# Performance work log

Measured on AMD Instinct MI355X. Metric: run time of the kernel, lower is better.

Reference implementation:

```python
import jax, jax.numpy as jnp
import numpy as np

N_RAYS = 65536
N_COARSE = 64
N_FINE = 128


def setup_inputs() -> dict:
    key = jax.random.key(0)
    k0, k1, k2 = jax.random.split(key, 3)
    origins = jax.random.normal(k0, (N_RAYS, 3), dtype=jnp.float32)
    directions = jax.random.normal(k1, (N_RAYS, 3), dtype=jnp.float32)
    near = jnp.full((N_RAYS,), 2.0, dtype=jnp.float32)
    far = jnp.full((N_RAYS,), 6.0, dtype=jnp.float32)
    # coarse-pass weights used for inverse-CDF (PDF) fine sampling
    weights = jax.random.uniform(k2, (N_RAYS, N_COARSE), dtype=jnp.float32)
    return {"origins": origins, "directions": directions, "near": near,
            "far": far, "weights": weights}


def sample_pdf(bins, weights, n_samples):
    """Inverse-CDF sampling. bins: [N, B], weights: [N, B-1] -> [N, n_samples]."""
    w = weights + 1e-5                       # avoid nans / empty bins
    pdf = w / jnp.sum(w, axis=-1, keepdims=True)
    cdf = jnp.cumsum(pdf, axis=-1)
    cdf = jnp.concatenate([jnp.zeros_like(cdf[..., :1]), cdf], axis=-1)  # [N, B]
    # deterministic (perturb=False) uniform samples in [0, 1]
    u = jnp.linspace(0.0, 1.0, n_samples, dtype=cdf.dtype)
    u = jnp.broadcast_to(u, cdf.shape[:-1] + (n_samples,))
    inds = jax.vmap(lambda c, uu: jnp.searchsorted(c, uu, side="right"))(cdf, u)
    below = jnp.clip(inds - 1, 0, cdf.shape[-1] - 1)
    above = jnp.clip(inds, 0, cdf.shape[-1] - 1)
    cdf_b = jnp.take_along_axis(cdf, below, axis=-1)
    cdf_a = jnp.take_along_axis(cdf, above, axis=-1)
    bins_b = jnp.take_along_axis(bins, below, axis=-1)
    bins_a = jnp.take_along_axis(bins, above, axis=-1)
    denom = cdf_a - cdf_b
    denom = jnp.where(denom < 1e-5, jnp.ones_like(denom), denom)
    t = (u - cdf_b) / denom
    return bins_b + t * (bins_a - bins_b)


def reference(origins, directions, near, far, weights):
    # normalize ray directions (RayBundle.__post_init__)
    directions = directions / jnp.linalg.norm(directions, axis=-1, keepdims=True)
    # stratified coarse depths (uniform in depth, perturb=False)
    t = jnp.linspace(0.0, 1.0, N_COARSE, dtype=origins.dtype)
    z_coarse = near[:, None] + (far - near)[:, None] * t          # [N, 64]
    # hierarchical PDF sampling on interval midpoints (NeRF convention)
    mids = 0.5 * (z_coarse[:, 1:] + z_coarse[:, :-1])             # [N, 63]
    z_fine = sample_pdf(mids, weights[:, 1:-1], N_FINE)           # [N, 128]
    # merge + sort by depth (RaySamples.merge / sort_by_depth)
    z = jnp.sort(jnp.concatenate([z_coarse, z_fine], axis=-1), axis=-1)  # [N, 192]
    positions = origins[:, None, :] + z[..., None] * directions[:, None, :]
    view_directions = jnp.broadcast_to(directions[:, None, :], positions.shape)
    d = jnp.diff(z, axis=-1)
    deltas = jnp.concatenate([d, d[:, -1:]], axis=-1)             # last delta repeats
    return positions, view_directions, z, deltas
```

## Files before the change

kernel.cpp:

```cpp
#include <hip/hip_runtime.h>

#define NR 65536
#define RPB 4

typedef float f32x4 __attribute__((ext_vector_type(4)));

__device__ __forceinline__ float coarse_at(int j, float nr, float dnf) {
    return fmaf((float)j * (1.0f / 63.0f), dnf, nr);
}

__global__ __launch_bounds__(256) void ray_sampler_kernel(
    const float* __restrict__ origins,
    const float* __restrict__ directions,
    const float* __restrict__ nearv,
    const float* __restrict__ farv,
    const float* __restrict__ weights,
    float* __restrict__ out)
{
    __shared__ float s_cdf[RPB][64];
    __shared__ float s_fine[RPB][128];
    __shared__ float s_z[RPB][192];
    __shared__ float s_pos[RPB][576];
    __shared__ float s_vd[RPB][16];

    const int tid  = threadIdx.x;
    const int wv   = tid >> 6;
    const int lane = tid & 63;
    const int r    = blockIdx.x * RPB + wv;

    const float nr  = nearv[r];
    const float fr  = farv[r];
    const float dnf = fr - nr;

    float dx = directions[3*r+0];
    float dy = directions[3*r+1];
    float dz = directions[3*r+2];
    const float invn = 1.0f / sqrtf(dx*dx + dy*dy + dz*dz);
    dx *= invn; dy *= invn; dz *= invn;
    const float ox = origins[3*r+0];
    const float oy = origins[3*r+1];
    const float oz = origins[3*r+2];

    if (lane < 12) {
        const int c = lane % 3;
        s_vd[wv][lane] = (c == 0) ? dx : ((c == 1) ? dy : dz);
    }

    float w = 0.0f;
    if (lane < 62) w = weights[(size_t)r*64 + lane + 1] + 1e-5f;
    float sc = w;
    #pragma unroll
    for (int off = 1; off < 64; off <<= 1) {
        float t = __shfl_up(sc, off, 64);
        if (lane >= off) sc += t;
    }
    const float total = __shfl(sc, 63, 64);
    const float invT  = 1.0f / total;
    if (lane < 62) s_cdf[wv][lane + 1] = sc * invT;
    if (lane == 62) s_cdf[wv][0] = 0.0f;

    const float* cdf = s_cdf[wv];
    float fval0, fval1;
    #pragma unroll
    for (int sIt = 0; sIt < 2; ++sIt) {
        const int s = lane + sIt * 64;
        const float u = (float)s * (1.0f/127.0f);
        int lo = 0, hi = 63;
        #pragma unroll
        for (int it = 0; it < 6; ++it) {
            if (lo < hi) {
                int mid = (lo + hi) >> 1;
                if (cdf[mid] <= u) lo = mid + 1; else hi = mid;
            }
        }
        int below = lo - 1; below = below < 0 ? 0 : (below > 62 ? 62 : below);
        int above = lo > 62 ? 62 : lo;
        const float cb = cdf[below], ca = cdf[above];
        const float bb = fmaf(((float)below + 0.5f) * (1.0f/63.0f), dnf, nr);
        const float ba = fmaf(((float)above + 0.5f) * (1.0f/63.0f), dnf, nr);
        float den = ca - cb;
        if (den < 1e-5f) den = 1.0f;
        const float tt = (u - cb) / den;
        const float fv = bb + tt * (ba - bb);
        s_fine[wv][s] = fv;
        if (sIt == 0) fval0 = fv; else fval1 = fv;
    }

    const float* fine = s_fine[wv];
    {
        const float v = coarse_at(lane, nr, dnf);
        int lo = 0, hi = 128;
        #pragma unroll
        for (int it = 0; it < 8; ++it) {
            if (lo < hi) {
                int mid = (lo + hi) >> 1;
                if (fine[mid] < v) lo = mid + 1; else hi = mid;
            }
        }
        s_z[wv][lane + lo] = v;
    }
    #pragma unroll
    for (int sIt = 0; sIt < 2; ++sIt) {
        const float v = (sIt == 0) ? fval0 : fval1;
        int lo = 0, hi = 64;
        #pragma unroll
        for (int it = 0; it < 7; ++it) {
            if (lo < hi) {
                int mid = (lo + hi) >> 1;
                if (coarse_at(mid, nr, dnf) <= v) lo = mid + 1; else hi = mid;
            }
        }
        s_z[wv][lane + sIt * 64 + lo] = v;
    }

    const float* zm = s_z[wv];
    float* posb = out + (size_t)r * 576;
    float* vdb  = out + (size_t)NR * 576  + (size_t)r * 576;
    float* zb   = out + (size_t)NR * 1152 + (size_t)r * 192;
    float* dlb  = out + (size_t)NR * 1344 + (size_t)r * 192;

    #pragma unroll
    for (int ri = 0; ri < 3; ++ri) {
        const int k  = lane + ri * 64;
        const float zz = zm[k];
        const int kn = (k == 191) ? 190 : (k + 1);
        const float zn = zm[kn];
        const float dl = fabsf(zn - zz);
        s_pos[wv][3*k + 0] = fmaf(zz, dx, ox);
        s_pos[wv][3*k + 1] = fmaf(zz, dy, oy);
        s_pos[wv][3*k + 2] = fmaf(zz, dz, oz);
        __builtin_nontemporal_store(zz, zb + k);
        __builtin_nontemporal_store(dl, dlb + k);
    }

    int l3 = lane % 3;
    const f32x4* posp = reinterpret_cast<const f32x4*>(s_pos[wv]);
    const f32x4* vdp  = reinterpret_cast<const f32x4*>(s_vd[wv]);
    f32x4* pos4 = reinterpret_cast<f32x4*>(posb);
    f32x4* vd4  = reinterpret_cast<f32x4*>(vdb);
    #pragma unroll
    for (int qi = 0; qi < 2; ++qi) {
        const int q = lane + qi * 64;
        int p = l3 + qi; p -= (p >= 3) ? 3 : 0;
        __builtin_nontemporal_store(posp[q], pos4 + q);
        __builtin_nontemporal_store(vdp[p],  vd4 + q);
    }
    if (lane < 16) {
        const int q = 128 + lane;
        int p = l3 + 2; p -= (p >= 3) ? 3 : 0;
        __builtin_nontemporal_store(posp[q], pos4 + q);
        __builtin_nontemporal_store(vdp[p],  vd4 + q);
    }
}

extern "C" void kernel_launch(void* const* d_in, const int* in_sizes, int n_in,
                              void* d_out, int out_size, void* d_ws, size_t ws_size,
                              hipStream_t stream) {
    const float* origins    = (const float*)d_in[0];
    const float* directions = (const float*)d_in[1];
    const float* nearv      = (const float*)d_in[2];
    const float* farv       = (const float*)d_in[3];
    const float* weights    = (const float*)d_in[4];
    float* out = (float*)d_out;

    dim3 grid(NR / RPB);
    dim3 block(256);
    ray_sampler_kernel<<<grid, block, 0, stream>>>(origins, directions, nearv, farv, weights, out);
}
```

Baseline: 81.56 us.

## Use DPP scan, keep CDF bounds from search, compute positions directly without LDS staging

Replaces the shuffle-based prefix scan with DPP row shifts and broadcasts plus readlane. The CDF binary search now tracks its bracketing values, so the two follow-up LDS reads are gone. The shared position and view-direction buffers are removed: each lane computes its float4 of positions and view directions directly from two z values. The z and delta outputs are written as float4 stores by 48 lanes. Together these cut LDS traffic and scalar stores, at the cost of more index arithmetic per lane and reliance on the DPP control encodings being correct.

```diff
diff --git a/kernel.cpp b/kernel.cpp
--- a/kernel.cpp
+++ b/kernel.cpp
@@ -4,6 +4,13 @@
 #define RPB 4
 
 typedef float f32x4 __attribute__((ext_vector_type(4)));
+
+#define SCAN_STEP(ctrl, rmask)                                                  \
+    do {                                                                        \
+        int _t = __builtin_amdgcn_update_dpp(0, __float_as_int(sc),             \
+                                             (ctrl), (rmask), 0xf, true);       \
+        sc += __int_as_float(_t);                                               \
+    } while (0)
 
 __device__ __forceinline__ float coarse_at(int j, float nr, float dnf) {
     return fmaf((float)j * (1.0f / 63.0f), dnf, nr);
@@ -20,8 +27,6 @@
     __shared__ float s_cdf[RPB][64];
     __shared__ float s_fine[RPB][128];
     __shared__ float s_z[RPB][192];
-    __shared__ float s_pos[RPB][576];
-    __shared__ float s_vd[RPB][16];
 
     const int tid  = threadIdx.x;
     const int wv   = tid >> 6;
@@ -29,8 +34,7 @@
     const int r    = blockIdx.x * RPB + wv;
 
     const float nr  = nearv[r];
-    const float fr  = farv[r];
-    const float dnf = fr - nr;
+    const float dnf = farv[r] - nr;
 
     float dx = directions[3*r+0];
     float dy = directions[3*r+1];
@@ -41,49 +45,47 @@
     const float oy = origins[3*r+1];
     const float oz = origins[3*r+2];
 
-    if (lane < 12) {
-        const int c = lane % 3;
-        s_vd[wv][lane] = (c == 0) ? dx : ((c == 1) ? dy : dz);
-    }
-
     float w = 0.0f;
     if (lane < 62) w = weights[(size_t)r*64 + lane + 1] + 1e-5f;
     float sc = w;
-    #pragma unroll
-    for (int off = 1; off < 64; off <<= 1) {
-        float t = __shfl_up(sc, off, 64);
-        if (lane >= off) sc += t;
-    }
-    const float total = __shfl(sc, 63, 64);
+    SCAN_STEP(0x111, 0xf);
+    SCAN_STEP(0x112, 0xf);
+    SCAN_STEP(0x114, 0xf);
+    SCAN_STEP(0x118, 0xf);
+    SCAN_STEP(0x142, 0xa);
+    SCAN_STEP(0x143, 0xc);
+    const float total = __int_as_float(__builtin_amdgcn_readlane(__float_as_int(sc), 63));
     const float invT  = 1.0f / total;
     if (lane < 62) s_cdf[wv][lane + 1] = sc * invT;
     if (lane == 62) s_cdf[wv][0] = 0.0f;
 
     const float* cdf = s_cdf[wv];
-    float fval0, fval1;
+    float fv0, fv1;
     #pragma unroll
     for (int sIt = 0; sIt < 2; ++sIt) {
         const int s = lane + sIt * 64;
         const float u = (float)s * (1.0f/127.0f);
         int lo = 0, hi = 63;
+        float vb = 0.0f, va = 1.0f;
         #pragma unroll
         for (int it = 0; it < 6; ++it) {
             if (lo < hi) {
-                int mid = (lo + hi) >> 1;
-                if (cdf[mid] <= u) lo = mid + 1; else hi = mid;
+                const int mid = (lo + hi) >> 1;
+                const float m = cdf[mid];
+                if (m <= u) { lo = mid + 1; vb = m; }
+                else        { hi = mid;     va = m; }
             }
         }
-        int below = lo - 1; below = below < 0 ? 0 : (below > 62 ? 62 : below);
-        int above = lo > 62 ? 62 : lo;
-        const float cb = cdf[below], ca = cdf[above];
+        const int below = (lo > 0) ? lo - 1 : 0;
+        const int above = (lo > 62) ? 62 : lo;
         const float bb = fmaf(((float)below + 0.5f) * (1.0f/63.0f), dnf, nr);
         const float ba = fmaf(((float)above + 0.5f) * (1.0f/63.0f), dnf, nr);
-        float den = ca - cb;
+        float den = va - vb;
         if (den < 1e-5f) den = 1.0f;
-        const float tt = (u - cb) / den;
+        const float tt = (u - vb) / den;
         const float fv = bb + tt * (ba - bb);
         s_fine[wv][s] = fv;
-        if (sIt == 0) fval0 = fv; else fval1 = fv;
+        if (sIt == 0) fv0 = fv; else fv1 = fv;
     }
 
     const float* fine = s_fine[wv];
@@ -93,7 +95,7 @@
         #pragma unroll
         for (int it = 0; it < 8; ++it) {
             if (lo < hi) {
-                int mid = (lo + hi) >> 1;
+                const int mid = (lo + hi) >> 1;
                 if (fine[mid] < v) lo = mid + 1; else hi = mid;
             }
         }
@@ -101,55 +103,61 @@
     }
     #pragma unroll
     for (int sIt = 0; sIt < 2; ++sIt) {
-        const float v = (sIt == 0) ? fval0 : fval1;
+        const float v = (sIt == 0) ? fv0 : fv1;
         int lo = 0, hi = 64;
         #pragma unroll
         for (int it = 0; it < 7; ++it) {
             if (lo < hi) {
-                int mid = (lo + hi) >> 1;
+                const int mid = (lo + hi) >> 1;
                 if (coarse_at(mid, nr, dnf) <= v) lo = mid + 1; else hi = mid;
             }
         }
         s_z[wv][lane + sIt * 64 + lo] = v;
     }
 
-    const float* zm = s_z[wv];
+    const float* zw = s_z[wv];
     float* posb = out + (size_t)r * 576;
     float* vdb  = out + (size_t)NR * 576  + (size_t)r * 576;
     float* zb   = out + (size_t)NR * 1152 + (size_t)r * 192;
     float* dlb  = out + (size_t)NR * 1344 + (size_t)r * 192;
 
-    #pragma unroll
-    for (int ri = 0; ri < 3; ++ri) {
-        const int k  = lane + ri * 64;
-        const float zz = zm[k];
-        const int kn = (k == 191) ? 190 : (k + 1);
-        const float zn = zm[kn];
-        const float dl = fabsf(zn - zz);
-        s_pos[wv][3*k + 0] = fmaf(zz, dx, ox);
-        s_pos[wv][3*k + 1] = fmaf(zz, dy, oy);
-        s_pos[wv][3*k + 2] = fmaf(zz, dz, oz);
-        __builtin_nontemporal_store(zz, zb + k);
-        __builtin_nontemporal_store(dl, dlb + k);
+    if (lane < 48) {
+        const f32x4 zq = *reinterpret_cast<const f32x4*>(&zw[4 * lane]);
+        const int nx = (lane == 47) ? 190 : (4 * lane + 4);
+        const float znx = zw[nx];
+        f32x4 dl;
+        dl[0] = zq[1] - zq[0];
+        dl[1] = zq[2] - zq[1];
+        dl[2] = zq[3] - zq[2];
+        dl[3] = (lane == 47) ? (zq[3] - zq[2]) : (znx - zq[3]);
+        __builtin_nontemporal_store(zq, reinterpret_cast<f32x4*>(zb) + lane);
+        __builtin_nontemporal_store(dl, reinterpret_cast<f32x4*>(dlb) + lane);
     }
 
-    int l3 = lane % 3;
-    const f32x4* posp = reinterpret_cast<const f32x4*>(s_pos[wv]);
-    const f32x4* vdp  = reinterpret_cast<const f32x4*>(s_vd[wv]);
     f32x4* pos4 = reinterpret_cast<f32x4*>(posb);
     f32x4* vd4  = reinterpret_cast<f32x4*>(vdb);
+    const int l3 = lane % 3;
     #pragma unroll
-    for (int qi = 0; qi < 2; ++qi) {
-        const int q = lane + qi * 64;
-        int p = l3 + qi; p -= (p >= 3) ? 3 : 0;
-        __builtin_nontemporal_store(posp[q], pos4 + q);
-        __builtin_nontemporal_store(vdp[p],  vd4 + q);
-    }
-    if (lane < 16) {
-        const int q = 128 + lane;
-        int p = l3 + 2; p -= (p >= 3) ? 3 : 0;
-        __builtin_nontemporal_store(posp[q], pos4 + q);
-        __builtin_nontemporal_store(vdp[p],  vd4 + q);
+    for (int qi = 0; qi < 3; ++qi) {
+        if (qi < 2 || lane < 16) {
+            const int q = lane + qi * 64;
+            int p = l3 + qi; p -= (p >= 3) ? 3 : 0;
+            const int k0 = (4 * q - p) / 3;
+            const float z0 = zw[k0];
+            const float z1 = zw[k0 + 1];
+            f32x4 pv, vv;
+            #pragma unroll
+            for (int m = 0; m < 4; ++m) {
+                int c = p + m; c -= (c >= 3) ? 3 : 0;
+                const float dc = (c == 0) ? dx : ((c == 1) ? dy : dz);
+                const float oc = (c == 0) ? ox : ((c == 1) ? oy : oz);
+                const float zz = (p + m >= 3) ? z1 : z0;
+                pv[m] = fmaf(zz, dc, oc);
+                vv[m] = dc;
+            }
+            __builtin_nontemporal_store(pv, pos4 + q);
+            __builtin_nontemporal_store(vv, vd4 + q);
+        }
     }
 }
 
```

After: 81.75 us. Within noise of the previous version (+0.2%).
